# Kernel optimization log

Measured on AMD Instinct MI355X. Metric: run time of the kernel, lower is better.

Reference implementation:

```python
import jax, jax.numpy as jnp
import numpy as np

H, HKV, D, W = 16, 4, 128, 1024   # n_head, n_kv_head, head_dim, sliding_window_size
NE = 2048                          # n_embd
QMAX = 3.0                         # 3-bit symmetric uniform quant: codes in [-3, 3]


def _rope(x, cos, sin):
    # x: [B,T,h,D]; cos/sin: [1,T,1,D//2]
    d = x.shape[-1] // 2
    x1, x2 = x[..., :d], x[..., d:]
    return jnp.concatenate([x1 * cos + x2 * sin, -x1 * sin + x2 * cos], axis=-1)


def _rmsnorm(x):
    eps = jnp.asarray(jnp.finfo(x.dtype).eps, x.dtype)  # F.rms_norm default eps
    return x * jax.lax.rsqrt(jnp.mean(x * x, axis=-1, keepdims=True) + eps)


def _quant_dequant(x):
    # Per-(B,H,t) token symmetric uniform 3-bit scalar quantization over head_dim,
    # matching QuantizedKVCache(head_dim, bits=3): codes * scale round-trip.
    s = jnp.max(jnp.abs(x), axis=-1, keepdims=True) / QMAX
    s = jnp.maximum(s, jnp.asarray(1e-8, x.dtype))
    codes = jnp.clip(jnp.round(x / s), -QMAX, QMAX)
    return codes * s


def setup_inputs() -> dict:
    key = jax.random.key(0)
    ks = jax.random.split(key, 5)
    B, T = 1, 4096
    x = jax.random.normal(ks[0], (B, T, NE), jnp.float32)
    half = D // 2
    inv = 1.0 / (10000.0 ** (np.arange(half, dtype=np.float64) / half))
    ang = np.arange(T)[:, None] * inv[None, :]
    cos = jnp.asarray(np.cos(ang), jnp.float32)[None, :, None, :]  # [1,T,1,D/2]
    sin = jnp.asarray(np.sin(ang), jnp.float32)[None, :, None, :]
    std = 0.02
    Wq = std * jax.random.normal(ks[1], (NE, H * D), jnp.float32)
    Wk = std * jax.random.normal(ks[2], (NE, HKV * D), jnp.float32)
    Wv = std * jax.random.normal(ks[3], (NE, HKV * D), jnp.float32)
    Wo = std * jax.random.normal(ks[4], (NE, NE), jnp.float32)
    return {"x": x, "cos": cos, "sin": sin, "Wq": Wq, "Wk": Wk, "Wv": Wv, "Wo": Wo}


def reference(x, cos, sin, Wq, Wk, Wv, Wo):
    B, T, C = x.shape
    q = (x @ Wq).reshape(B, T, H, D)
    k = (x @ Wk).reshape(B, T, HKV, D)
    v = (x @ Wv).reshape(B, T, HKV, D)
    q = _rmsnorm(_rope(q, cos, sin))
    k = _rmsnorm(_rope(k, cos, sin))
    rep = H // HKV  # GQA: repeat each kv head consecutively
    k = jnp.repeat(k, rep, axis=2)
    v = jnp.repeat(v, rep, axis=2)
    q = q.transpose(0, 2, 1, 3)  # [B,H,T,D]
    k = k.transpose(0, 2, 1, 3)
    v = v.transpose(0, 2, 1, 3)
    # 3-bit quantize-dequantize KV (element-wise round trip, T > W path)
    kq = _quant_dequant(k)
    vq = _quant_dequant(v)
    nc = T // W  # number of query chunks
    KW = 2 * W - 1  # window length per chunk (kv_start = start - W + 1 .. end)
    # pad front by W-1 so every chunk's window starts at padded index chunk*W
    kp = jnp.pad(kq, ((0, 0), (0, 0), (W - 1, 0), (0, 0)))
    vp = jnp.pad(vq, ((0, 0), (0, 0), (W - 1, 0), (0, 0)))
    idx = (jnp.arange(nc) * W)[:, None] + jnp.arange(KW)[None, :]  # [nc,KW]
    kw = kp[:, :, idx]  # [B,H,nc,KW,D]
    vw = vp[:, :, idx]
    qc = q.reshape(B, H, nc, W, D)
    scale = 1.0 / np.sqrt(D)  # yarn_scale=1.0
    scores = jnp.einsum('bhcqd,bhckd->bhcqk', qc, kw) * scale  # [B,H,nc,W,KW]
    # sliding-window causal mask per chunk
    ql = jnp.arange(W)[:, None]            # local query pos
    kl = jnp.arange(KW)[None, :]           # local key pos in window
    dist = ql - kl + (W - 1)               # q_abs - k_abs
    valid = (dist >= 0) & (dist < W)       # [W,KW]
    kabs = (jnp.arange(nc) * W)[:, None] - (W - 1) + jnp.arange(KW)[None, :]  # [nc,KW]
    valid = valid[None, :, :] & (kabs[:, None, :] >= 0)  # [nc,W,KW] (drop pad)
    scores = jnp.where(valid[None, None], scores, -jnp.inf)
    attn = jax.nn.softmax(scores, axis=-1)
    out = jnp.einsum('bhcqk,bhckd->bhcqd', attn, vw)  # [B,H,nc,W,D]
    y = out.reshape(B, H, T, D).transpose(0, 2, 1, 3).reshape(B, T, C)
    return y @ Wo
```

## Files before the change

kernel.cpp:

```cpp
#include <hip/hip_runtime.h>
#include <hip/hip_bf16.h>
#include <math.h>

#define T_SEQ 4096
#define NEMB  2048
#define NH    16
#define NKV   4
#define HD    128
#define WIN   1024

typedef __attribute__((ext_vector_type(8))) __bf16 bf16x8;
typedef __attribute__((ext_vector_type(4))) float  f32x4;

__device__ __forceinline__ float wave_sum64(float v) {
#pragma unroll
  for (int off = 1; off < 64; off <<= 1) v += __shfl_xor(v, off, 64);
  return v;
}
__device__ __forceinline__ float wave_max64(float v) {
#pragma unroll
  for (int off = 1; off < 64; off <<= 1) v = fmaxf(v, __shfl_xor(v, off, 64));
  return v;
}

__global__ __launch_bounds__(256) void cast_x_split_kernel(const float* __restrict__ src,
                                                           __bf16* __restrict__ dst) {
  int i = blockIdx.x * 256 + threadIdx.x;
  int row = i >> 8, colg = i & 255;
  const f32x4* s4 = (const f32x4*)src;
  f32x4 a = s4[2 * i], b = s4[2 * i + 1];
  bf16x8 hi, lo;
#pragma unroll
  for (int j = 0; j < 4; ++j) {
    hi[j] = (__bf16)a[j]; lo[j] = (__bf16)(a[j] - (float)hi[j]);
    hi[j + 4] = (__bf16)b[j]; lo[j + 4] = (__bf16)(b[j] - (float)hi[j + 4]);
  }
  *(bf16x8*)(dst + (size_t)row * 4096 + colg * 8) = hi;
  *(bf16x8*)(dst + (size_t)row * 4096 + 2048 + colg * 8) = lo;
}

__global__ __launch_bounds__(64) void transpose_cast_kernel(const float* __restrict__ src,
                                                            __bf16* __restrict__ dst,
                                                            int K, int N) {
  int kc = blockIdx.x * 8;
  int n  = blockIdx.y * 64 + threadIdx.x;
  bf16x8 o;
#pragma unroll
  for (int j = 0; j < 8; ++j) o[j] = (__bf16)src[(size_t)(kc + j) * N + n];
  *(bf16x8*)(dst + (size_t)n * K + kc) = o;
}

__global__ __launch_bounds__(64) void transpose_split_kernel(const float* __restrict__ src,
                                                             __bf16* __restrict__ dst,
                                                             int N) {
  int kc = blockIdx.x * 8;
  int n  = blockIdx.y * 64 + threadIdx.x;
  bf16x8 hi, lo;
#pragma unroll
  for (int j = 0; j < 8; ++j) {
    float v = src[(size_t)(kc + j) * N + n];
    hi[j] = (__bf16)v; lo[j] = (__bf16)(v - (float)hi[j]);
  }
  *(bf16x8*)(dst + (size_t)n * 6144 + kc) = hi;
  *(bf16x8*)(dst + (size_t)n * 6144 + 2048 + kc) = hi;
  *(bf16x8*)(dst + (size_t)n * 6144 + 4096 + kc) = lo;
}

template <bool OUT_BF16>
__global__ __launch_bounds__(256) void gemm_kernel(const __bf16* __restrict__ A,
                                                   const __bf16* __restrict__ BT,
                                                   void* __restrict__ Cout,
                                                   int M, int N, int K,
                                                   int lda, int ldb, int awrap) {
  __shared__ bf16x8 As[1024];
  __shared__ bf16x8 Bs[1024];
  const int tid = threadIdx.x;
  const int lane = tid & 63, w = tid >> 6;
  const int wr = w >> 1, wc = w & 1;
  const int g = lane >> 4, c = lane & 15;
  const int m0 = blockIdx.y * 128, n0 = blockIdx.x * 128;
  const int rs = tid >> 3, cs = tid & 7;
  f32x4 acc[4][4] = {};
  for (int k0 = 0; k0 < K; k0 += 64) {
    int ka = k0 + cs * 8;
    int kaw = (ka >= awrap) ? ka - awrap : ka;
    __syncthreads();
#pragma unroll
    for (int i = 0; i < 4; ++i) {
      int row = rs + 32 * i;
      As[row * 8 + (cs ^ (row & 7))] = *(const bf16x8*)(A  + (size_t)(m0 + row) * lda + kaw);
      Bs[row * 8 + (cs ^ (row & 7))] = *(const bf16x8*)(BT + (size_t)(n0 + row) * ldb + ka);
    }
    __syncthreads();
#pragma unroll
    for (int kk = 0; kk < 2; ++kk) {
      bf16x8 af[4], bfr[4];
#pragma unroll
      for (int mi = 0; mi < 4; ++mi) {
        int row = wr * 64 + mi * 16 + c;
        af[mi] = As[row * 8 + ((kk * 4 + g) ^ (row & 7))];
      }
#pragma unroll
      for (int ni = 0; ni < 4; ++ni) {
        int row = wc * 64 + ni * 16 + c;
        bfr[ni] = Bs[row * 8 + ((kk * 4 + g) ^ (row & 7))];
      }
#pragma unroll
      for (int mi = 0; mi < 4; ++mi)
#pragma unroll
        for (int ni = 0; ni < 4; ++ni)
          acc[mi][ni] = __builtin_amdgcn_mfma_f32_16x16x32_bf16(af[mi], bfr[ni], acc[mi][ni], 0, 0, 0);
    }
  }
#pragma unroll
  for (int mi = 0; mi < 4; ++mi) {
#pragma unroll
    for (int ni = 0; ni < 4; ++ni) {
      int row = m0 + wr * 64 + mi * 16 + g * 4;
      int col = n0 + wc * 64 + ni * 16 + c;
#pragma unroll
      for (int r = 0; r < 4; ++r) {
        if constexpr (OUT_BF16)
          ((__bf16*)Cout)[(size_t)(row + r) * N + col] = (__bf16)acc[mi][ni][r];
        else
          ((float*)Cout)[(size_t)(row + r) * N + col] = acc[mi][ni][r];
      }
    }
  }
}

__global__ __launch_bounds__(256) void rope_norm_quant_kernel(const __bf16* __restrict__ qproj,
                                                              const float* __restrict__ kvproj,
                                                              const float* __restrict__ cosp,
                                                              const float* __restrict__ sinp,
                                                              __bf16* __restrict__ qb,
                                                              __bf16* __restrict__ kb,
                                                              __bf16* __restrict__ vt) {
  const int t = blockIdx.x;
  const int w = threadIdx.x >> 6, lane = threadIdx.x & 63;
  const int slot = blockIdx.y * 4 + w;
  float a, b;
  if (slot < 16) {
    const __bf16* base = qproj + (size_t)t * 2048 + slot * 128;
    a = (float)base[lane]; b = (float)base[lane + 64];
  } else {
    const float* base = kvproj + (size_t)t * 1024 + (slot - 16) * 128;
    a = base[lane]; b = base[lane + 64];
  }
  float o1, o2;
  if (slot < 20) {
    float cv = cosp[t * 64 + lane], sv = sinp[t * 64 + lane];
    o1 = a * cv + b * sv;
    o2 = -a * sv + b * cv;
    float ss = wave_sum64(o1 * o1 + o2 * o2);
    float sc = rsqrtf(ss * (1.0f / 128.0f) + 1.1920929e-7f);
    o1 *= sc; o2 *= sc;
  } else { o1 = a; o2 = b; }
  if (slot < 16) {
    __bf16* dst = qb + ((size_t)slot * T_SEQ + t) * HD;
    dst[lane] = (__bf16)o1; dst[lane + 64] = (__bf16)o2;
  } else {
    float amax = wave_max64(fmaxf(fabsf(o1), fabsf(o2)));
    float s = fmaxf(amax * (1.0f / 3.0f), 1e-8f);
    float d1 = fminf(fmaxf(rintf(o1 / s), -3.0f), 3.0f) * s;
    float d2 = fminf(fmaxf(rintf(o2 / s), -3.0f), 3.0f) * s;
    if (slot < 20) {
      __bf16* dst = kb + ((size_t)(slot - 16) * T_SEQ + t) * HD;
      dst[lane] = (__bf16)d1; dst[lane + 64] = (__bf16)d2;
    } else {
      __bf16* dst = vt + (size_t)(slot - 20) * HD * T_SEQ;
      dst[(size_t)lane * T_SEQ + t]        = (__bf16)d1;
      dst[(size_t)(lane + 64) * T_SEQ + t] = (__bf16)d2;
    }
  }
}

__global__ __launch_bounds__(256) void attn_kernel(const __bf16* __restrict__ qb,
                                                   const __bf16* __restrict__ kb,
                                                   const __bf16* __restrict__ vt,
                                                   __bf16* __restrict__ attn) {
  __shared__ __align__(16) __bf16 plds[4][32][40];
  const int w = threadIdx.x >> 6, lane = threadIdx.x & 63;
  const int g = lane >> 4, c = lane & 15;
  const int wg = blockIdx.x * 4 + w;
  const int h = wg >> 7, qt = wg & 127;
  const int q0 = qt * 32;
  const int hkv = h >> 2;
  const __bf16* kbase = kb + (size_t)hkv * T_SEQ * HD;
  const __bf16* vbase = vt + (size_t)hkv * HD * T_SEQ;
  const float scl = 0.08838834764831845f;

  bf16x8 qf[2][4];
#pragma unroll
  for (int mi = 0; mi < 2; ++mi)
#pragma unroll
    for (int kc = 0; kc < 4; ++kc)
      qf[mi][kc] = *(const bf16x8*)(qb + ((size_t)h * T_SEQ + q0 + 16 * mi + c) * HD + kc * 32 + 8 * g);

  f32x4 acc[2][8] = {};
  float lsum[2][4] = {};

  int lo = q0 - (WIN - 1);
  if (lo < 0) lo = 0;
  lo &= ~31;
  for (int kj0 = lo; kj0 <= q0 + 31; kj0 += 32) {
    f32x4 s[2][2] = {};
#pragma unroll
    for (int kc = 0; kc < 4; ++kc) {
      bf16x8 bk0 = *(const bf16x8*)(kbase + (size_t)(kj0 + c) * HD + kc * 32 + 8 * g);
      bf16x8 bk1 = *(const bf16x8*)(kbase + (size_t)(kj0 + 16 + c) * HD + kc * 32 + 8 * g);
#pragma unroll
      for (int mi = 0; mi < 2; ++mi) {
        s[mi][0] = __builtin_amdgcn_mfma_f32_16x16x32_bf16(qf[mi][kc], bk0, s[mi][0], 0, 0, 0);
        s[mi][1] = __builtin_amdgcn_mfma_f32_16x16x32_bf16(qf[mi][kc], bk1, s[mi][1], 0, 0, 0);
      }
    }
    float p[2][2][4];
#pragma unroll
    for (int mi = 0; mi < 2; ++mi)
#pragma unroll
      for (int ni = 0; ni < 2; ++ni)
#pragma unroll
        for (int r = 0; r < 4; ++r) {
          int qrow = q0 + 16 * mi + 4 * g + r;
          int kcol = kj0 + 16 * ni + c;
          int d = qrow - kcol;
          float e = __expf(s[mi][ni][r] * scl);
          p[mi][ni][r] = (d >= 0 && d < WIN) ? e : 0.0f;
        }
#pragma unroll
    for (int mi = 0; mi < 2; ++mi)
#pragma unroll
      for (int r = 0; r < 4; ++r)
        lsum[mi][r] += p[mi][0][r] + p[mi][1][r];
#pragma unroll
    for (int mi = 0; mi < 2; ++mi)
#pragma unroll
      for (int ni = 0; ni < 2; ++ni)
#pragma unroll
        for (int r = 0; r < 4; ++r)
          plds[w][16 * mi + 4 * g + r][16 * ni + c] = (__bf16)p[mi][ni][r];
    asm volatile("s_waitcnt lgkmcnt(0)" ::: "memory");
    __builtin_amdgcn_sched_barrier(0);
    bf16x8 pa[2];
#pragma unroll
    for (int mi = 0; mi < 2; ++mi) pa[mi] = *(const bf16x8*)&plds[w][16 * mi + c][8 * g];
#pragma unroll
    for (int df = 0; df < 8; ++df) {
      bf16x8 bv = *(const bf16x8*)(vbase + (size_t)(df * 16 + c) * T_SEQ + kj0 + 8 * g);
#pragma unroll
      for (int mi = 0; mi < 2; ++mi)
        acc[mi][df] = __builtin_amdgcn_mfma_f32_16x16x32_bf16(pa[mi], bv, acc[mi][df], 0, 0, 0);
    }
    asm volatile("" ::: "memory");
  }
#pragma unroll
  for (int mi = 0; mi < 2; ++mi) {
#pragma unroll
    for (int off = 1; off < 16; off <<= 1)
#pragma unroll
      for (int r = 0; r < 4; ++r) lsum[mi][r] += __shfl_xor(lsum[mi][r], off, 64);
    float inv[4];
#pragma unroll
    for (int r = 0; r < 4; ++r) inv[r] = 1.0f / lsum[mi][r];
#pragma unroll
    for (int df = 0; df < 8; ++df)
#pragma unroll
      for (int r = 0; r < 4; ++r) {
        float v = acc[mi][df][r] * inv[r];
        attn[(size_t)(q0 + 16 * mi + 4 * g + r) * NEMB + h * HD + df * 16 + c] = (__bf16)v;
      }
  }
}

extern "C" void kernel_launch(void* const* d_in, const int* in_sizes, int n_in,
                              void* d_out, int out_size, void* d_ws, size_t ws_size,
                              hipStream_t stream) {
  (void)in_sizes; (void)n_in; (void)out_size; (void)ws_size;
  const float* x    = (const float*)d_in[0];
  const float* cosp = (const float*)d_in[1];
  const float* sinp = (const float*)d_in[2];
  const float* Wq   = (const float*)d_in[3];
  const float* Wk   = (const float*)d_in[4];
  const float* Wv   = (const float*)d_in[5];
  const float* Wo   = (const float*)d_in[6];

  char* ws = (char*)d_ws;
  __bf16* xsplit = (__bf16*)(ws + 0);
  __bf16* qproj  = (__bf16*)(ws + 33554432);
  float*  kvproj = (float*)(ws + 50331648);
  __bf16* wqT    = (__bf16*)(ws + 67108864);
  __bf16* wkvT   = (__bf16*)(ws + 75497472);
  __bf16* wot    = (__bf16*)(ws + 88080384);
  __bf16* qbuf   = (__bf16*)(ws + 96468992);
  __bf16* kbuf   = (__bf16*)(ws + 113246208);
  __bf16* vbuf   = (__bf16*)(ws + 117440512);
  __bf16* abuf   = (__bf16*)(ws + 0);

  cast_x_split_kernel<<<4096, 256, 0, stream>>>(x, xsplit);
  transpose_cast_kernel<<<dim3(256, 32), 64, 0, stream>>>(Wq, wqT, 2048, 2048);
  transpose_split_kernel<<<dim3(256, 8), 64, 0, stream>>>(Wk, wkvT, 512);
  transpose_split_kernel<<<dim3(256, 8), 64, 0, stream>>>(Wv, wkvT + (size_t)512 * 6144, 512);
  transpose_cast_kernel<<<dim3(256, 32), 64, 0, stream>>>(Wo, wot, 2048, 2048);

  gemm_kernel<true><<<dim3(16, 32), 256, 0, stream>>>(xsplit, wqT, qproj,
                                                      4096, 2048, 2048, 4096, 2048, 1 << 30);
  gemm_kernel<false><<<dim3(8, 32), 256, 0, stream>>>(xsplit, wkvT, kvproj,
                                                      4096, 1024, 6144, 4096, 6144, 4096);
  rope_norm_quant_kernel<<<dim3(4096, 6), 256, 0, stream>>>(qproj, kvproj, cosp, sinp,
                                                            qbuf, kbuf, vbuf);
  attn_kernel<<<512, 256, 0, stream>>>(qbuf, kbuf, vbuf, abuf);
  gemm_kernel<false><<<dim3(16, 32), 256, 0, stream>>>(abuf, wot, d_out,
                                                       4096, 2048, 2048, 2048, 2048, 1 << 30);
}
```

Baseline: 517.0 us.

## Split attention KV range across two waves and use direct-to-LDS loads in GEMM

The attention kernel now gives each 32-query tile its own 128-thread block. The two waves each process half of the sliding-window key range, then the partial outputs and row sums are combined through shared memory. This doubles the number of waves and shortens each wave's serial loop, at the cost of an LDS reduction and a block barrier. Separately, the GEMM stages A/B tiles with global_load_lds straight into an unswizzled row-major LDS layout. That removes the register round-trip, but the fragment reads may now hit LDS bank conflicts.

```diff
diff --git a/kernel.cpp b/kernel.cpp
--- a/kernel.cpp
+++ b/kernel.cpp
@@ -11,6 +11,11 @@
 
 typedef __attribute__((ext_vector_type(8))) __bf16 bf16x8;
 typedef __attribute__((ext_vector_type(4))) float  f32x4;
+
+#define GLOAD_LDS16(gp, lp)                                          \
+  __builtin_amdgcn_global_load_lds(                                  \
+      (const __attribute__((address_space(1))) void*)(gp),           \
+      (__attribute__((address_space(3))) void*)(lp), 16, 0, 0)
 
 __device__ __forceinline__ float wave_sum64(float v) {
 #pragma unroll
@@ -72,39 +77,37 @@
                                                    void* __restrict__ Cout,
                                                    int M, int N, int K,
                                                    int lda, int ldb, int awrap) {
-  __shared__ bf16x8 As[1024];
-  __shared__ bf16x8 Bs[1024];
+  __shared__ __align__(16) __bf16 As[128 * 64];
+  __shared__ __align__(16) __bf16 Bs[128 * 64];
   const int tid = threadIdx.x;
   const int lane = tid & 63, w = tid >> 6;
   const int wr = w >> 1, wc = w & 1;
   const int g = lane >> 4, c = lane & 15;
   const int m0 = blockIdx.y * 128, n0 = blockIdx.x * 128;
-  const int rs = tid >> 3, cs = tid & 7;
+  const int srow = lane >> 3;
+  const int scol = lane & 7;
   f32x4 acc[4][4] = {};
   for (int k0 = 0; k0 < K; k0 += 64) {
-    int ka = k0 + cs * 8;
+    int ka = k0 + scol * 8;
     int kaw = (ka >= awrap) ? ka - awrap : ka;
     __syncthreads();
 #pragma unroll
     for (int i = 0; i < 4; ++i) {
-      int row = rs + 32 * i;
-      As[row * 8 + (cs ^ (row & 7))] = *(const bf16x8*)(A  + (size_t)(m0 + row) * lda + kaw);
-      Bs[row * 8 + (cs ^ (row & 7))] = *(const bf16x8*)(BT + (size_t)(n0 + row) * ldb + ka);
+      int chunk = w * 4 + i;
+      int row = chunk * 8 + srow;
+      GLOAD_LDS16(A  + (size_t)(m0 + row) * lda + kaw, As + chunk * 512);
+      GLOAD_LDS16(BT + (size_t)(n0 + row) * ldb + ka,  Bs + chunk * 512);
     }
     __syncthreads();
 #pragma unroll
     for (int kk = 0; kk < 2; ++kk) {
       bf16x8 af[4], bfr[4];
 #pragma unroll
-      for (int mi = 0; mi < 4; ++mi) {
-        int row = wr * 64 + mi * 16 + c;
-        af[mi] = As[row * 8 + ((kk * 4 + g) ^ (row & 7))];
-      }
-#pragma unroll
-      for (int ni = 0; ni < 4; ++ni) {
-        int row = wc * 64 + ni * 16 + c;
-        bfr[ni] = Bs[row * 8 + ((kk * 4 + g) ^ (row & 7))];
-      }
+      for (int mi = 0; mi < 4; ++mi)
+        af[mi] = *(const bf16x8*)&As[(wr * 64 + mi * 16 + c) * 64 + (kk * 4 + g) * 8];
+#pragma unroll
+      for (int ni = 0; ni < 4; ++ni)
+        bfr[ni] = *(const bf16x8*)&Bs[(wc * 64 + ni * 16 + c) * 64 + (kk * 4 + g) * 8];
 #pragma unroll
       for (int mi = 0; mi < 4; ++mi)
 #pragma unroll
@@ -175,15 +178,17 @@
   }
 }
 
-__global__ __launch_bounds__(256) void attn_kernel(const __bf16* __restrict__ qb,
+__global__ __launch_bounds__(128) void attn_kernel(const __bf16* __restrict__ qb,
                                                    const __bf16* __restrict__ kb,
                                                    const __bf16* __restrict__ vt,
                                                    __bf16* __restrict__ attn) {
-  __shared__ __align__(16) __bf16 plds[4][32][40];
+  __shared__ __align__(16) __bf16 plds[2][32][40];
+  __shared__ __align__(16) float comb[128][36];
+  __shared__ __align__(16) float lsumL[32];
   const int w = threadIdx.x >> 6, lane = threadIdx.x & 63;
   const int g = lane >> 4, c = lane & 15;
-  const int wg = blockIdx.x * 4 + w;
-  const int h = wg >> 7, qt = wg & 127;
+  const int tile = blockIdx.x;
+  const int h = tile >> 7, qt = tile & 127;
   const int q0 = qt * 32;
   const int hkv = h >> 2;
   const __bf16* kbase = kb + (size_t)hkv * T_SEQ * HD;
@@ -203,7 +208,12 @@
   int lo = q0 - (WIN - 1);
   if (lo < 0) lo = 0;
   lo &= ~31;
-  for (int kj0 = lo; kj0 <= q0 + 31; kj0 += 32) {
+  const int nst = (q0 - lo) / 32 + 1;
+  const int nh = nst >> 1;
+  const int s0 = w ? nh : 0;
+  const int s1 = w ? nst : nh;
+  for (int si = s0; si < s1; ++si) {
+    const int kj0 = lo + si * 32;
     f32x4 s[2][2] = {};
 #pragma unroll
     for (int kc = 0; kc < 4; ++kc) {
@@ -255,21 +265,43 @@
     asm volatile("" ::: "memory");
   }
 #pragma unroll
-  for (int mi = 0; mi < 2; ++mi) {
+  for (int mi = 0; mi < 2; ++mi)
 #pragma unroll
     for (int off = 1; off < 16; off <<= 1)
 #pragma unroll
       for (int r = 0; r < 4; ++r) lsum[mi][r] += __shfl_xor(lsum[mi][r], off, 64);
-    float inv[4];
-#pragma unroll
-    for (int r = 0; r < 4; ++r) inv[r] = 1.0f / lsum[mi][r];
-#pragma unroll
-    for (int df = 0; df < 8; ++df)
-#pragma unroll
-      for (int r = 0; r < 4; ++r) {
-        float v = acc[mi][df][r] * inv[r];
-        attn[(size_t)(q0 + 16 * mi + 4 * g + r) * NEMB + h * HD + df * 16 + c] = (__bf16)v;
+  if (w == 1) {
+#pragma unroll
+    for (int mi = 0; mi < 2; ++mi) {
+#pragma unroll
+      for (int df = 0; df < 8; ++df)
+        *(f32x4*)&comb[df * 16 + c][16 * mi + 4 * g] = acc[mi][df];
+      if (c == 0) {
+        f32x4 t;
+#pragma unroll
+        for (int r = 0; r < 4; ++r) t[r] = lsum[mi][r];
+        *(f32x4*)&lsumL[16 * mi + 4 * g] = t;
       }
+    }
+  }
+  __syncthreads();
+  if (w == 0) {
+#pragma unroll
+    for (int mi = 0; mi < 2; ++mi) {
+      f32x4 lw = *(const f32x4*)&lsumL[16 * mi + 4 * g];
+      float inv[4];
+#pragma unroll
+      for (int r = 0; r < 4; ++r) inv[r] = 1.0f / (lsum[mi][r] + lw[r]);
+#pragma unroll
+      for (int df = 0; df < 8; ++df) {
+        f32x4 cv = *(const f32x4*)&comb[df * 16 + c][16 * mi + 4 * g];
+#pragma unroll
+        for (int r = 0; r < 4; ++r) {
+          float v = (acc[mi][df][r] + cv[r]) * inv[r];
+          attn[(size_t)(q0 + 16 * mi + 4 * g + r) * NEMB + h * HD + df * 16 + c] = (__bf16)v;
+        }
+      }
+    }
   }
 }
 
@@ -309,7 +341,7 @@
                                                       4096, 1024, 6144, 4096, 6144, 4096);
   rope_norm_quant_kernel<<<dim3(4096, 6), 256, 0, stream>>>(qproj, kvproj, cosp, sinp,
                                                             qbuf, kbuf, vbuf);
-  attn_kernel<<<512, 256, 0, stream>>>(qbuf, kbuf, vbuf, abuf);
+  attn_kernel<<<2048, 128, 0, stream>>>(qbuf, kbuf, vbuf, abuf);
   gemm_kernel<false><<<dim3(16, 32), 256, 0, stream>>>(abuf, wot, d_out,
                                                        4096, 2048, 2048, 2048, 2048, 1 << 30);
 }
```

Result: slower. 535.5 us (+3.6%).

## Use direct global-to-LDS GEMM loads and transposed register-only attention P exchange

Applied to the files above, without the earlier changes.

The GEMM now loads A/B tiles with global_load_lds (16-byte direct-to-LDS copies) instead of loading through registers and storing to shared memory, keeping the same XOR swizzle. The attention kernel computes S transposed (K as the A operand), which lets the P tile be repacked into the MFMA operand layout with cross-lane shuffles rather than a round-trip through LDS. It also prefetches V fragments at the top of each iteration and writes outputs as vectorised bf16x4 stores. This adds shuffle and select overhead and more live registers in exchange for removing LDS traffic and waits.

```diff
diff --git a/kernel.cpp b/kernel.cpp
--- a/kernel.cpp
+++ b/kernel.cpp
@@ -10,7 +10,13 @@
 #define WIN   1024
 
 typedef __attribute__((ext_vector_type(8))) __bf16 bf16x8;
+typedef __attribute__((ext_vector_type(4))) __bf16 bf16x4;
 typedef __attribute__((ext_vector_type(4))) float  f32x4;
+
+#define GLOAD_LDS16(gp, lp)                                          \
+  __builtin_amdgcn_global_load_lds(                                  \
+      (const __attribute__((address_space(1))) void*)(gp),           \
+      (__attribute__((address_space(3))) void*)(lp), 16, 0, 0)
 
 __device__ __forceinline__ float wave_sum64(float v) {
 #pragma unroll
@@ -21,6 +27,11 @@
 #pragma unroll
   for (int off = 1; off < 64; off <<= 1) v = fmaxf(v, __shfl_xor(v, off, 64));
   return v;
+}
+__device__ __forceinline__ uint32_t pack_bf16x2(float a, float b) {
+  union { __bf16 h[2]; uint32_t u; } u_;
+  u_.h[0] = (__bf16)a; u_.h[1] = (__bf16)b;
+  return u_.u;
 }
 
 __global__ __launch_bounds__(256) void cast_x_split_kernel(const float* __restrict__ src,
@@ -72,24 +83,26 @@
                                                    void* __restrict__ Cout,
                                                    int M, int N, int K,
                                                    int lda, int ldb, int awrap) {
-  __shared__ bf16x8 As[1024];
-  __shared__ bf16x8 Bs[1024];
+  __shared__ __align__(16) __bf16 As[128 * 64];
+  __shared__ __align__(16) __bf16 Bs[128 * 64];
   const int tid = threadIdx.x;
   const int lane = tid & 63, w = tid >> 6;
   const int wr = w >> 1, wc = w & 1;
   const int g = lane >> 4, c = lane & 15;
   const int m0 = blockIdx.y * 128, n0 = blockIdx.x * 128;
-  const int rs = tid >> 3, cs = tid & 7;
+  const int srow = lane >> 3;
+  const int sgrp = (lane & 7) ^ (srow & 7);
   f32x4 acc[4][4] = {};
   for (int k0 = 0; k0 < K; k0 += 64) {
-    int ka = k0 + cs * 8;
+    int ka = k0 + sgrp * 8;
     int kaw = (ka >= awrap) ? ka - awrap : ka;
     __syncthreads();
 #pragma unroll
     for (int i = 0; i < 4; ++i) {
-      int row = rs + 32 * i;
-      As[row * 8 + (cs ^ (row & 7))] = *(const bf16x8*)(A  + (size_t)(m0 + row) * lda + kaw);
-      Bs[row * 8 + (cs ^ (row & 7))] = *(const bf16x8*)(BT + (size_t)(n0 + row) * ldb + ka);
+      int chunk = w * 4 + i;
+      int row = chunk * 8 + srow;
+      GLOAD_LDS16(A  + (size_t)(m0 + row) * lda + kaw, As + chunk * 512);
+      GLOAD_LDS16(BT + (size_t)(n0 + row) * ldb + ka,  Bs + chunk * 512);
     }
     __syncthreads();
 #pragma unroll
@@ -98,12 +111,12 @@
 #pragma unroll
       for (int mi = 0; mi < 4; ++mi) {
         int row = wr * 64 + mi * 16 + c;
-        af[mi] = As[row * 8 + ((kk * 4 + g) ^ (row & 7))];
+        af[mi] = *(const bf16x8*)&As[row * 64 + (((kk * 4 + g) ^ (row & 7)) * 8)];
       }
 #pragma unroll
       for (int ni = 0; ni < 4; ++ni) {
         int row = wc * 64 + ni * 16 + c;
-        bfr[ni] = Bs[row * 8 + ((kk * 4 + g) ^ (row & 7))];
+        bfr[ni] = *(const bf16x8*)&Bs[row * 64 + (((kk * 4 + g) ^ (row & 7)) * 8)];
       }
 #pragma unroll
       for (int mi = 0; mi < 4; ++mi)
@@ -179,7 +192,6 @@
                                                    const __bf16* __restrict__ kb,
                                                    const __bf16* __restrict__ vt,
                                                    __bf16* __restrict__ attn) {
-  __shared__ __align__(16) __bf16 plds[4][32][40];
   const int w = threadIdx.x >> 6, lane = threadIdx.x & 63;
   const int g = lane >> 4, c = lane & 15;
   const int wg = blockIdx.x * 4 + w;
@@ -198,78 +210,80 @@
       qf[mi][kc] = *(const bf16x8*)(qb + ((size_t)h * T_SEQ + q0 + 16 * mi + c) * HD + kc * 32 + 8 * g);
 
   f32x4 acc[2][8] = {};
-  float lsum[2][4] = {};
+  float lsum[2] = {};
+
+  const int srcLow = ((g & 1) << 5) + c;
+  const int srcHigh = srcLow + 16;
+  const bool gHi = g >= 2;
 
   int lo = q0 - (WIN - 1);
   if (lo < 0) lo = 0;
   lo &= ~31;
   for (int kj0 = lo; kj0 <= q0 + 31; kj0 += 32) {
-    f32x4 s[2][2] = {};
+    bf16x8 vf[8];
+#pragma unroll
+    for (int df = 0; df < 8; ++df)
+      vf[df] = *(const bf16x8*)(vbase + (size_t)(df * 16 + c) * T_SEQ + kj0 + 8 * g);
+    f32x4 st[2][2] = {};
 #pragma unroll
     for (int kc = 0; kc < 4; ++kc) {
       bf16x8 bk0 = *(const bf16x8*)(kbase + (size_t)(kj0 + c) * HD + kc * 32 + 8 * g);
       bf16x8 bk1 = *(const bf16x8*)(kbase + (size_t)(kj0 + 16 + c) * HD + kc * 32 + 8 * g);
 #pragma unroll
       for (int mi = 0; mi < 2; ++mi) {
-        s[mi][0] = __builtin_amdgcn_mfma_f32_16x16x32_bf16(qf[mi][kc], bk0, s[mi][0], 0, 0, 0);
-        s[mi][1] = __builtin_amdgcn_mfma_f32_16x16x32_bf16(qf[mi][kc], bk1, s[mi][1], 0, 0, 0);
+        st[0][mi] = __builtin_amdgcn_mfma_f32_16x16x32_bf16(bk0, qf[mi][kc], st[0][mi], 0, 0, 0);
+        st[1][mi] = __builtin_amdgcn_mfma_f32_16x16x32_bf16(bk1, qf[mi][kc], st[1][mi], 0, 0, 0);
       }
     }
     float p[2][2][4];
 #pragma unroll
+    for (int ni = 0; ni < 2; ++ni)
+#pragma unroll
+      for (int mi = 0; mi < 2; ++mi)
+#pragma unroll
+        for (int r = 0; r < 4; ++r) {
+          int qrow = q0 + 16 * mi + c;
+          int key = kj0 + 16 * ni + 4 * g + r;
+          int d = qrow - key;
+          float e = __expf(st[ni][mi][r] * scl);
+          p[ni][mi][r] = (d >= 0 && d < WIN) ? e : 0.0f;
+        }
+#pragma unroll
     for (int mi = 0; mi < 2; ++mi)
-#pragma unroll
-      for (int ni = 0; ni < 2; ++ni)
-#pragma unroll
-        for (int r = 0; r < 4; ++r) {
-          int qrow = q0 + 16 * mi + 4 * g + r;
-          int kcol = kj0 + 16 * ni + c;
-          int d = qrow - kcol;
-          float e = __expf(s[mi][ni][r] * scl);
-          p[mi][ni][r] = (d >= 0 && d < WIN) ? e : 0.0f;
-        }
-#pragma unroll
-    for (int mi = 0; mi < 2; ++mi)
-#pragma unroll
-      for (int r = 0; r < 4; ++r)
-        lsum[mi][r] += p[mi][0][r] + p[mi][1][r];
-#pragma unroll
-    for (int mi = 0; mi < 2; ++mi)
-#pragma unroll
-      for (int ni = 0; ni < 2; ++ni)
-#pragma unroll
-        for (int r = 0; r < 4; ++r)
-          plds[w][16 * mi + 4 * g + r][16 * ni + c] = (__bf16)p[mi][ni][r];
-    asm volatile("s_waitcnt lgkmcnt(0)" ::: "memory");
-    __builtin_amdgcn_sched_barrier(0);
-    bf16x8 pa[2];
-#pragma unroll
-    for (int mi = 0; mi < 2; ++mi) pa[mi] = *(const bf16x8*)&plds[w][16 * mi + c][8 * g];
+      lsum[mi] += (p[0][mi][0] + p[0][mi][1] + p[0][mi][2] + p[0][mi][3]) +
+                  (p[1][mi][0] + p[1][mi][1] + p[1][mi][2] + p[1][mi][3]);
+#pragma unroll
+    for (int mi = 0; mi < 2; ++mi) {
+      uint32_t pk00 = pack_bf16x2(p[0][mi][0], p[0][mi][1]);
+      uint32_t pk01 = pack_bf16x2(p[0][mi][2], p[0][mi][3]);
+      uint32_t pk10 = pack_bf16x2(p[1][mi][0], p[1][mi][1]);
+      uint32_t pk11 = pack_bf16x2(p[1][mi][2], p[1][mi][3]);
+      uint32_t n0a = __shfl((int)pk00, srcLow),  n0b = __shfl((int)pk01, srcLow);
+      uint32_t n0c = __shfl((int)pk00, srcHigh), n0d = __shfl((int)pk01, srcHigh);
+      uint32_t n1a = __shfl((int)pk10, srcLow),  n1b = __shfl((int)pk11, srcLow);
+      uint32_t n1c = __shfl((int)pk10, srcHigh), n1d = __shfl((int)pk11, srcHigh);
+      union { uint32_t u[4]; bf16x8 v; } bu;
+      bu.u[0] = gHi ? n1a : n0a;
+      bu.u[1] = gHi ? n1b : n0b;
+      bu.u[2] = gHi ? n1c : n0c;
+      bu.u[3] = gHi ? n1d : n0d;
+#pragma unroll
+      for (int df = 0; df < 8; ++df)
+        acc[mi][df] = __builtin_amdgcn_mfma_f32_16x16x32_bf16(vf[df], bu.v, acc[mi][df], 0, 0, 0);
+    }
+  }
+#pragma unroll
+  for (int mi = 0; mi < 2; ++mi) {
+    lsum[mi] += __shfl_xor(lsum[mi], 16, 64);
+    lsum[mi] += __shfl_xor(lsum[mi], 32, 64);
+    float inv = 1.0f / lsum[mi];
 #pragma unroll
     for (int df = 0; df < 8; ++df) {
-      bf16x8 bv = *(const bf16x8*)(vbase + (size_t)(df * 16 + c) * T_SEQ + kj0 + 8 * g);
-#pragma unroll
-      for (int mi = 0; mi < 2; ++mi)
-        acc[mi][df] = __builtin_amdgcn_mfma_f32_16x16x32_bf16(pa[mi], bv, acc[mi][df], 0, 0, 0);
-    }
-    asm volatile("" ::: "memory");
-  }
-#pragma unroll
-  for (int mi = 0; mi < 2; ++mi) {
-#pragma unroll
-    for (int off = 1; off < 16; off <<= 1)
-#pragma unroll
-      for (int r = 0; r < 4; ++r) lsum[mi][r] += __shfl_xor(lsum[mi][r], off, 64);
-    float inv[4];
-#pragma unroll
-    for (int r = 0; r < 4; ++r) inv[r] = 1.0f / lsum[mi][r];
-#pragma unroll
-    for (int df = 0; df < 8; ++df)
-#pragma unroll
-      for (int r = 0; r < 4; ++r) {
-        float v = acc[mi][df][r] * inv[r];
-        attn[(size_t)(q0 + 16 * mi + 4 * g + r) * NEMB + h * HD + df * 16 + c] = (__bf16)v;
-      }
+      bf16x4 o;
+#pragma unroll
+      for (int r = 0; r < 4; ++r) o[r] = (__bf16)(acc[mi][df][r] * inv);
+      *(bf16x4*)(attn + (size_t)(q0 + 16 * mi + c) * NEMB + h * HD + df * 16 + 4 * g) = o;
+    }
   }
 }
 
```

Result: no change. 514.4 us (-0.5%).
